# Optimization experiments

Measured on AMD Instinct MI355X. Metric: run time of the kernel, lower is better.

## Reference

```python
import jax, jax.numpy as jnp
import numpy as np

DIM = 512
DIM_EDGES = 64
LN_EPS = 1e-5


def setup_inputs() -> dict:
    key = jax.random.key(0)
    ks = jax.random.split(key, 4)
    b, n = 2, 768
    x = jax.random.normal(ks[0], (b, n, DIM), dtype=jnp.float32)
    # nn.Linear weights stored as [out, in], applied as x @ W.T
    W_rows = jax.random.normal(ks[1], (DIM_EDGES, DIM), dtype=jnp.float32) / np.sqrt(DIM)
    W_cols = jax.random.normal(ks[2], (DIM_EDGES, DIM), dtype=jnp.float32) / np.sqrt(DIM)
    W_edges = jax.random.normal(ks[3], (DIM_EDGES, DIM_EDGES), dtype=jnp.float32) / np.sqrt(DIM_EDGES)
    ln_gamma = jnp.ones((DIM_EDGES,), dtype=jnp.float32)
    ln_beta = jnp.zeros((DIM_EDGES,), dtype=jnp.float32)
    return {"x": x, "W_rows": W_rows, "W_cols": W_cols, "W_edges": W_edges,
            "ln_gamma": ln_gamma, "ln_beta": ln_beta}


def reference(x, W_rows, W_cols, W_edges, ln_gamma, ln_beta):
    # rows/cols: [b, n, d_e]
    rows = jnp.einsum('bnd,ed->bne', x, W_rows)
    cols = jnp.einsum('bnd,ed->bne', x, W_cols)
    # outer sum: [b, i, j, d_e]
    outer = rows[:, :, None, :] + cols[:, None, :, :]
    # edge linear (no bias): [b, i, j, d_e]
    h = jnp.einsum('bije,fe->bijf', outer, W_edges)
    # LayerNorm over last dim
    mu = jnp.mean(h, axis=-1, keepdims=True)
    var = jnp.mean(jnp.square(h - mu), axis=-1, keepdims=True)
    out = (h - mu) * jax.lax.rsqrt(var + LN_EPS) * ln_gamma + ln_beta
    return out
```

## Files before the change

kernel.cpp:

```cpp
#include <hip/hip_runtime.h>

#define B 2
#define N 768
#define DIM 512
#define DE 64
#define LN_EPS 1e-5f

#define OFF_RC   0
#define OFF_CC   (B*N*DE)
#define OFF_SSR  (2*B*N*DE)
#define OFF_SSC  (2*B*N*DE + B*N)

__global__ __launch_bounds__(256) void ee_precompute(
    const float* __restrict__ x, const float* __restrict__ Wr,
    const float* __restrict__ Wc, const float* __restrict__ We,
    float* __restrict__ Rc, float* __restrict__ Cc,
    float* __restrict__ ssqR, float* __restrict__ ssqC)
{
    __shared__ float xs[DIM];
    __shared__ float rc[2 * DE];

    const int tok = blockIdx.x;
    const int tid = threadIdx.x;
    const int lane = tid & 63;
    const int wave = tid >> 6;

    const float* xp = x + (size_t)tok * DIM;
    xs[tid]       = xp[tid];
    xs[tid + 256] = xp[tid + 256];
    __syncthreads();

    const float4 b0 = *(const float4*)(xs + lane * 8);
    const float4 b1 = *(const float4*)(xs + lane * 8 + 4);
    for (int m = 0; m < 32; ++m) {
        const int o = wave * 32 + m;
        const float* W = (o < DE) ? (Wr + (size_t)o * DIM)
                                  : (Wc + (size_t)(o - DE) * DIM);
        const float4 a0 = *(const float4*)(W + lane * 8);
        const float4 a1 = *(const float4*)(W + lane * 8 + 4);
        float p = a0.x*b0.x + a0.y*b0.y + a0.z*b0.z + a0.w*b0.w
                + a1.x*b1.x + a1.y*b1.y + a1.z*b1.z + a1.w*b1.w;
        #pragma unroll
        for (int s = 1; s < 64; s <<= 1) p += __shfl_xor(p, s);
        if (lane == 0) rc[o] = p;
    }
    __syncthreads();

    if (tid < 128) {
        const int f = lane;
        const float* W = We + (size_t)f * DE;
        const float* rcp = (wave == 0) ? rc : (rc + DE);
        float acc = 0.f;
        #pragma unroll
        for (int e4 = 0; e4 < DE / 4; ++e4) {
            const float4 w4 = *(const float4*)(W + e4 * 4);
            const float4 r4 = *(const float4*)(rcp + e4 * 4);
            acc += w4.x*r4.x + w4.y*r4.y + w4.z*r4.z + w4.w*r4.w;
        }
        float mu = acc;
        #pragma unroll
        for (int s = 1; s < 64; s <<= 1) mu += __shfl_xor(mu, s);
        mu *= (1.f / DE);
        const float c = acc - mu;
        float sq = c * c;
        #pragma unroll
        for (int s = 1; s < 64; s <<= 1) sq += __shfl_xor(sq, s);
        float* dst = ((wave == 0) ? Rc : Cc) + (size_t)tok * DE;
        dst[f] = c;
        if (lane == 0) ((wave == 0) ? ssqR : ssqC)[tok] = sq;
    }
}

__global__ __launch_bounds__(256) void ee_outer_ln(
    const float* __restrict__ Rc, const float* __restrict__ Cc,
    const float* __restrict__ ssqRp, const float* __restrict__ ssqCp,
    const float* __restrict__ gamma, const float* __restrict__ beta,
    float* __restrict__ out)
{
    const int bi = blockIdx.x;
    const int tid = threadIdx.x;
    const int lane = tid & 63;
    const int wave = tid >> 6;
    const int jsub = lane >> 4;
    const int fb = (lane & 15) * 4;

    const int b = bi / N;
    const float* Ccb   = Cc + (size_t)b * N * DE;
    const float* ssqCb = ssqCp + (size_t)b * N;
    float* outb = out + (size_t)bi * N * DE;

    const float ssqR = ssqRp[bi];
    const float4 r  = *(const float4*)(Rc + (size_t)bi * DE + fb);
    const float4 g  = *(const float4*)(gamma + fb);
    const float4 be = *(const float4*)(beta + fb);

    for (int t = 0; t < N / 16; ++t) {
        const int j = t * 16 + wave * 4 + jsub;
        const float4 c = *(const float4*)(Ccb + (size_t)j * DE + fb);
        const float ssqC = ssqCb[j];

        float p = r.x*c.x + r.y*c.y + r.z*c.z + r.w*c.w;
        p += __shfl_xor(p, 1);
        p += __shfl_xor(p, 2);
        p += __shfl_xor(p, 4);
        p += __shfl_xor(p, 8);

        const float var = (ssqR + ssqC + 2.f * p) * (1.f / DE);
        const float s = rsqrtf(var + LN_EPS);

        float4 o;
        o.x = (r.x + c.x) * (s * g.x) + be.x;
        o.y = (r.y + c.y) * (s * g.y) + be.y;
        o.z = (r.z + c.z) * (s * g.z) + be.z;
        o.w = (r.w + c.w) * (s * g.w) + be.w;
        *(float4*)(outb + (size_t)j * DE + fb) = o;
    }
}

extern "C" void kernel_launch(void* const* d_in, const int* in_sizes, int n_in,
                              void* d_out, int out_size, void* d_ws, size_t ws_size,
                              hipStream_t stream) {
    const float* x     = (const float*)d_in[0];
    const float* Wr    = (const float*)d_in[1];
    const float* Wc    = (const float*)d_in[2];
    const float* We    = (const float*)d_in[3];
    const float* gamma = (const float*)d_in[4];
    const float* beta  = (const float*)d_in[5];
    float* out = (float*)d_out;
    float* ws  = (float*)d_ws;

    float* Rc   = ws + OFF_RC;
    float* Cc   = ws + OFF_CC;
    float* ssqR = ws + OFF_SSR;
    float* ssqC = ws + OFF_SSC;

    ee_precompute<<<B * N, 256, 0, stream>>>(x, Wr, Wc, We, Rc, Cc, ssqR, ssqC);
    ee_outer_ln<<<B * N, 256, 0, stream>>>(Rc, Cc, ssqR, ssqC, gamma, beta, out);
}
```

Before: 342.6 us.

## Batch four tokens per precompute block and use nontemporal stores for output

```diff
diff --git a/kernel.cpp b/kernel.cpp
--- a/kernel.cpp
+++ b/kernel.cpp
@@ -5,6 +5,9 @@
 #define DIM 512
 #define DE 64
 #define LN_EPS 1e-5f
+#define TPB 4
+
+typedef float v4f __attribute__((ext_vector_type(4)));
 
 #define OFF_RC   0
 #define OFF_CC   (B*N*DE)
@@ -17,39 +20,59 @@
     float* __restrict__ Rc, float* __restrict__ Cc,
     float* __restrict__ ssqR, float* __restrict__ ssqC)
 {
-    __shared__ float xs[DIM];
-    __shared__ float rc[2 * DE];
+    __shared__ float xs[TPB * DIM];
+    __shared__ float rc[TPB][2 * DE];
 
-    const int tok = blockIdx.x;
+    const int tok0 = blockIdx.x * TPB;
     const int tid = threadIdx.x;
     const int lane = tid & 63;
     const int wave = tid >> 6;
 
-    const float* xp = x + (size_t)tok * DIM;
-    xs[tid]       = xp[tid];
-    xs[tid + 256] = xp[tid + 256];
+    const float* xp = x + (size_t)tok0 * DIM;
+    #pragma unroll
+    for (int k = 0; k < TPB * DIM / 256; ++k)
+        xs[tid + k * 256] = xp[tid + k * 256];
     __syncthreads();
 
-    const float4 b0 = *(const float4*)(xs + lane * 8);
-    const float4 b1 = *(const float4*)(xs + lane * 8 + 4);
+    float4 xb[TPB][2];
+    #pragma unroll
+    for (int tt = 0; tt < TPB; ++tt) {
+        xb[tt][0] = *(const float4*)(xs + tt * DIM + lane * 8);
+        xb[tt][1] = *(const float4*)(xs + tt * DIM + lane * 8 + 4);
+    }
+
     for (int m = 0; m < 32; ++m) {
         const int o = wave * 32 + m;
         const float* W = (o < DE) ? (Wr + (size_t)o * DIM)
                                   : (Wc + (size_t)(o - DE) * DIM);
         const float4 a0 = *(const float4*)(W + lane * 8);
         const float4 a1 = *(const float4*)(W + lane * 8 + 4);
-        float p = a0.x*b0.x + a0.y*b0.y + a0.z*b0.z + a0.w*b0.w
-                + a1.x*b1.x + a1.y*b1.y + a1.z*b1.z + a1.w*b1.w;
+        float p[TPB];
         #pragma unroll
-        for (int s = 1; s < 64; s <<= 1) p += __shfl_xor(p, s);
-        if (lane == 0) rc[o] = p;
+        for (int tt = 0; tt < TPB; ++tt) {
+            p[tt] = a0.x*xb[tt][0].x + a0.y*xb[tt][0].y
+                  + a0.z*xb[tt][0].z + a0.w*xb[tt][0].w
+                  + a1.x*xb[tt][1].x + a1.y*xb[tt][1].y
+                  + a1.z*xb[tt][1].z + a1.w*xb[tt][1].w;
+        }
+        #pragma unroll
+        for (int s = 1; s < 64; s <<= 1) {
+            #pragma unroll
+            for (int tt = 0; tt < TPB; ++tt) p[tt] += __shfl_xor(p[tt], s);
+        }
+        if (lane == 0) {
+            #pragma unroll
+            for (int tt = 0; tt < TPB; ++tt) rc[tt][o] = p[tt];
+        }
     }
     __syncthreads();
 
-    if (tid < 128) {
-        const int f = lane;
-        const float* W = We + (size_t)f * DE;
-        const float* rcp = (wave == 0) ? rc : (rc + DE);
+    const int tt = wave;
+    const int f = lane;
+    const float* W = We + (size_t)f * DE;
+    #pragma unroll
+    for (int pass = 0; pass < 2; ++pass) {
+        const float* rcp = rc[tt] + pass * DE;
         float acc = 0.f;
         #pragma unroll
         for (int e4 = 0; e4 < DE / 4; ++e4) {
@@ -65,9 +88,9 @@
         float sq = c * c;
         #pragma unroll
         for (int s = 1; s < 64; s <<= 1) sq += __shfl_xor(sq, s);
-        float* dst = ((wave == 0) ? Rc : Cc) + (size_t)tok * DE;
+        float* dst = ((pass == 0) ? Rc : Cc) + (size_t)(tok0 + tt) * DE;
         dst[f] = c;
-        if (lane == 0) ((wave == 0) ? ssqR : ssqC)[tok] = sq;
+        if (lane == 0) ((pass == 0) ? ssqR : ssqC)[tok0 + tt] = sq;
     }
 }
 
@@ -94,6 +117,7 @@
     const float4 g  = *(const float4*)(gamma + fb);
     const float4 be = *(const float4*)(beta + fb);
 
+    #pragma unroll 2
     for (int t = 0; t < N / 16; ++t) {
         const int j = t * 16 + wave * 4 + jsub;
         const float4 c = *(const float4*)(Ccb + (size_t)j * DE + fb);
@@ -108,12 +132,12 @@
         const float var = (ssqR + ssqC + 2.f * p) * (1.f / DE);
         const float s = rsqrtf(var + LN_EPS);
 
-        float4 o;
+        v4f o;
         o.x = (r.x + c.x) * (s * g.x) + be.x;
         o.y = (r.y + c.y) * (s * g.y) + be.y;
         o.z = (r.z + c.z) * (s * g.z) + be.z;
         o.w = (r.w + c.w) * (s * g.w) + be.w;
-        *(float4*)(outb + (size_t)j * DE + fb) = o;
+        __builtin_nontemporal_store(o, (v4f*)(outb + (size_t)j * DE + fb));
     }
 }
 
@@ -134,6 +158,6 @@
     float* ssqR = ws + OFF_SSR;
     float* ssqC = ws + OFF_SSC;
 
-    ee_precompute<<<B * N, 256, 0, stream>>>(x, Wr, Wc, We, Rc, Cc, ssqR, ssqC);
+    ee_precompute<<<(B * N) / TPB, 256, 0, stream>>>(x, Wr, Wc, We, Rc, Cc, ssqR, ssqC);
     ee_outer_ln<<<B * N, 256, 0, stream>>>(Rc, Cc, ssqR, ssqC, gamma, beta, out);
 }
```

Result: slower. 349.9 us (+2.1%).
